# Kernel tuning notes

Hardware: AMD Instinct MI355X
Metric: run time of the kernel (lower is better)

## Reference

```python
import jax, jax.numpy as jnp
import numpy as np

BN = 128  # weight block rows
BK = 128  # quantization block along K
FP8_MAX = 448.0  # float8_e4m3fn max finite value
F8 = jnp.float8_e4m3fn


def _quant_dequant_act(x):
    # Dynamic per-token, per-128-block FP8 quantization (scale = amax/448), then dequant.
    M, K = x.shape
    xb = x.reshape(M, K // BK, BK)
    amax = jnp.max(jnp.abs(xb), axis=-1, keepdims=True)
    scale = jnp.maximum(amax, 1e-12) / FP8_MAX
    q = jnp.clip(xb / scale, -FP8_MAX, FP8_MAX).astype(F8)
    return (q.astype(jnp.float32) * scale).reshape(M, K)


def _dequant_weight(w, s):
    # w: (N, K) fp8, s: (N//BN, K//BK) f32 block scales
    N, K = w.shape
    sf = jnp.repeat(jnp.repeat(s, BN, axis=0), BK, axis=1)[:N, :K]
    return w.astype(jnp.float32) * sf


def _fp8_linear(x, w, s):
    # y = dequant(quant(x)) @ dequant(w)^T  -- matches w8a8_fp8_matmul semantics
    return _quant_dequant_act(x) @ _dequant_weight(w, s).T


def _quantize_weight(key, shape):
    E, N, K = shape
    w = jax.random.normal(key, shape, jnp.float32) * 0.02
    wb = w.reshape(E, N // BN, BN, K // BK, BK)
    amax = jnp.max(jnp.abs(wb), axis=(2, 4), keepdims=True)
    scale = jnp.maximum(amax, 1e-12) / FP8_MAX
    q = jnp.clip(wb / scale, -FP8_MAX, FP8_MAX).astype(F8).reshape(E, N, K)
    return q, scale.reshape(E, N // BN, K // BK)


def setup_inputs() -> dict:
    key = jax.random.key(0)
    k1, k2, k3, k4, k5 = jax.random.split(key, 5)
    T, H, I, E, TOPK = 2048, 2048, 1408, 8, 2
    hidden_states = jax.random.normal(k1, (T, H), jnp.float32)
    top_k_index = jax.random.randint(k2, (T, TOPK), 0, E).astype(jnp.int64)
    w = jax.random.uniform(k3, (T, TOPK), jnp.float32)
    top_k_weights = w / jnp.sum(w, axis=-1, keepdims=True)
    gate_up_proj, gate_up_proj_scale_inv = _quantize_weight(k4, (E, 2 * I, H))
    down_proj, down_proj_scale_inv = _quantize_weight(k5, (E, H, I))
    return {
        "hidden_states": hidden_states,
        "top_k_index": top_k_index,
        "top_k_weights": top_k_weights,
        "gate_up_proj": gate_up_proj,
        "gate_up_proj_scale_inv": gate_up_proj_scale_inv,
        "down_proj": down_proj,
        "down_proj_scale_inv": down_proj_scale_inv,
    }


def reference(hidden_states, top_k_index, top_k_weights, gate_up_proj,
              gate_up_proj_scale_inv, down_proj, down_proj_scale_inv):
    E = gate_up_proj.shape[0]
    I = down_proj.shape[-1]
    # Activation quantization is per-token: identical for every expert, compute once.
    x_dq = _quant_dequant_act(hidden_states)  # (T, H)
    out = jnp.zeros_like(hidden_states, dtype=jnp.float32)
    for e in range(E):  # fixed small expert loop (structural, not data dim)
        gu = x_dq @ _dequant_weight(gate_up_proj[e], gate_up_proj_scale_inv[e]).T  # (T, 2I)
        gate, up = gu[:, :I], gu[:, I:]
        h = jax.nn.silu(gate) * up
        d = _fp8_linear(h, down_proj[e], down_proj_scale_inv[e])  # (T, H)
        # routing weight for this expert per token (sums duplicates like index_add_)
        rw = jnp.sum(jnp.where(top_k_index == e, top_k_weights, 0.0), axis=-1)  # (T,)
        out = out + rw[:, None] * d
    return out.astype(hidden_states.dtype)
```

## Files before the change

kernel.cpp:

```cpp
#include <hip/hip_runtime.h>
#include <cstdint>
#include <cstddef>

using f32x4 = __attribute__((ext_vector_type(4))) float;

#define TDIM 2048
#define HDIM 2048
#define IDIM 1408
#define NEXP 8
#define NKB1 16
#define NKB2 11
#define MAXM 4096

__device__ __forceinline__ void gll16(const void* g, void* l) {
  __builtin_amdgcn_global_load_lds(
      (__attribute__((address_space(1))) void*)(uintptr_t)g,
      (__attribute__((address_space(3))) void*)(uint32_t)(uintptr_t)l,
      16, 0, 0);
}

__device__ __forceinline__ f32x4 mfma_fp8(long a, long b, f32x4 c) {
  return __builtin_amdgcn_mfma_f32_16x16x32_fp8_fp8(a, b, c, 0, 0, 0);
}

__device__ __forceinline__ uint32_t f8_1(float q) {
  q = fminf(fmaxf(q, -448.f), 448.f);
  return (uint32_t)__builtin_amdgcn_cvt_pk_fp8_f32(q, q, 0, false) & 0xffu;
}

__device__ __forceinline__ float bf16_to_f32(uint32_t bits16) {
  union { uint32_t u; float f; } c;
  c.u = bits16 << 16;
  return c.f;
}

__global__ void sniff_kernel(const uint16_t* __restrict__ a,
                             const uint16_t* __restrict__ b,
                             int* __restrict__ modes, int* __restrict__ cnt) {
  if (threadIdx.x < 8) cnt[threadIdx.x] = 0;
  if (threadIdx.x == 0) {
    unsigned acc = 0;
    for (int i = 0; i < 128; ++i) acc |= a[2 * i];
    modes[0] = (acc == 0) ? 1 : 0;
    acc = 0;
    for (int i = 0; i < 128; ++i) acc |= b[2 * i];
    modes[1] = (acc == 0) ? 1 : 0;
  }
}

__global__ void repack_kernel(const void* __restrict__ in, uint8_t* __restrict__ out,
                              int n8, const int* __restrict__ modes, int midx) {
  const int i = blockIdx.x * 256 + threadIdx.x;
  if (i >= n8) return;
  const int m = modes[midx];
  float f[8];
  if (m == 1) {
    const float4* p = (const float4*)in;
    float4 a = p[2 * i], b = p[2 * i + 1];
    f[0] = a.x; f[1] = a.y; f[2] = a.z; f[3] = a.w;
    f[4] = b.x; f[5] = b.y; f[6] = b.z; f[7] = b.w;
  } else {
    uint4 v = ((const uint4*)in)[i];
#pragma unroll
    for (int j = 0; j < 4; ++j) {
      uint32_t w = (&v.x)[j];
      f[2 * j]     = bf16_to_f32(w & 0xffffu);
      f[2 * j + 1] = bf16_to_f32(w >> 16);
    }
  }
  uint32_t lo = 0, hi = 0;
#pragma unroll
  for (int j = 0; j < 8; ++j) {
    uint32_t b8 = f8_1(f[j]);
    if (j < 4) lo |= b8 << (8 * j);
    else       hi |= b8 << (8 * (j - 4));
  }
  ((uint2*)out)[i] = make_uint2(lo, hi);
}

__global__ void quantx_kernel(const float* __restrict__ x,
                              uint8_t* __restrict__ xq, float* __restrict__ xs) {
  const int gid = blockIdx.x * 4 + (threadIdx.x >> 6);
  const int lane = threadIdx.x & 63;
  const int r = gid >> 4, kb = gid & 15;
  const float2 v = *(const float2*)(x + (size_t)r * HDIM + kb * 128 + lane * 2);
  float a = fmaxf(fabsf(v.x), fabsf(v.y));
#pragma unroll
  for (int d = 1; d < 64; d <<= 1) a = fmaxf(a, __shfl_xor(a, d));
  const float s = fmaxf(a, 1e-12f) / 448.f;
  const uint32_t b0 = f8_1(v.x / s);
  const uint32_t b1 = f8_1(v.y / s);
  *(uint16_t*)(xq + (size_t)r * HDIM + kb * 128 + lane * 2) = (uint16_t)(b0 | (b1 << 8));
  if (lane == 0) xs[r * 16 + kb] = s;
}

__global__ void route_kernel(const void* __restrict__ idxraw,
                             int* __restrict__ list, int* __restrict__ cnt) {
  const long long* p = (const long long*)idxraw;
  unsigned hi = 0;
#pragma unroll
  for (int j = 0; j < 16; ++j) hi |= (unsigned)((unsigned long long)p[j] >> 32);
  const int i = blockIdx.x * 256 + threadIdx.x;
  int e;
  if (hi == 0) {
    e = (int)p[i];
  } else {
    long long v = p[i >> 1];
    e = (int)((i & 1) ? (v >> 32) : (v & 0xffffffffLL));
  }
  e &= 7;
  const int pos = atomicAdd(&cnt[e], 1);
  list[e * MAXM + pos] = i;
}

__global__ __launch_bounds__(256) void gemm1_kernel(
    const uint8_t* __restrict__ xq, const float* __restrict__ xs,
    const uint8_t* __restrict__ w, const float* __restrict__ wscl,
    const int* __restrict__ list, const int* __restrict__ cnt,
    uint8_t* __restrict__ hq, float* __restrict__ hs) {
  const int e = blockIdx.z, mt = blockIdx.y, nb = blockIdx.x;
  const int M = cnt[e];
  if (mt * 64 >= M) return;
  __shared__ __align__(16) uint8_t As[8192];
  __shared__ __align__(16) uint8_t Bg[2 * 16384];
  __shared__ __align__(16) uint8_t Bu[2 * 16384];
  __shared__ int slots[64];
  __shared__ __align__(16) float sxsAll[16][64];
  __shared__ __align__(16) float amx[128];
  const int tid = threadIdx.x, lane = tid & 63, wid = tid >> 6;
  const int wr = wid >> 1, wc = wid & 1;
  if (tid < 64) {
    int m = mt * 64 + tid;
    slots[tid] = list[e * MAXM + (m < M ? m : 0)];
  }
  __syncthreads();
  {
    const int r = tid >> 2, q = tid & 3;
    const int tok = slots[r] >> 1;
    f32x4 v = *(const f32x4*)(xs + (size_t)tok * 16 + q * 4);
    sxsAll[q * 4 + 0][r] = v[0];
    sxsAll[q * 4 + 1][r] = v[1];
    sxsAll[q * 4 + 2][r] = v[2];
    sxsAll[q * 4 + 3][r] = v[3];
  }
  const int s = tid >> 3;
  const int cj0 = ((tid & 7) ^ (s & 7)) << 4;
  const long tokA0 = slots[s] >> 1;
  const long tokA1 = slots[s + 32] >> 1;
  const uint8_t* pA0 = xq + tokA0 * HDIM + cj0;
  const uint8_t* pA1 = xq + tokA1 * HDIM + cj0;
  const size_t wb = (size_t)e * (2 * IDIM) * HDIM;
  const uint8_t* pG = w + wb + (size_t)(nb * 128 + s) * HDIM + cj0;
  const uint8_t* pU = w + wb + (size_t)(IDIM + nb * 128 + s) * HDIM + cj0;
  const float* wsg = wscl + (size_t)e * 352 + nb * 16;
  const float* wsu = wsg + 176;
  f32x4 accg[2][4] = {};
  f32x4 accu[2][4] = {};
  const int kbyte = (lane >> 4) << 3;
#define STAGEB(d, kk) { const int ko_ = (kk) << 7; \
    _Pragma("unroll") \
    for (int k = 0; k < 4; ++k) { \
      gll16(pG + (size_t)(k * 32) * HDIM + ko_, Bg + (d) * 16384 + k * 4096 + tid * 16); \
      gll16(pU + (size_t)(k * 32) * HDIM + ko_, Bu + (d) * 16384 + k * 4096 + tid * 16); \
    } }
  f32x4 rA0 = *(const f32x4*)(pA0);
  f32x4 rA1 = *(const f32x4*)(pA1);
  STAGEB(0, 0)
  __syncthreads();
  int cur = 0;
  for (int kb = 0; kb < NKB1; ++kb) {
    *(f32x4*)(As + tid * 16) = rA0;
    *(f32x4*)(As + 4096 + tid * 16) = rA1;
    if (kb + 1 < NKB1) {
      STAGEB(cur ^ 1, kb + 1)
      const int ko = (kb + 1) << 7;
      rA0 = *(const f32x4*)(pA0 + ko);
      rA1 = *(const f32x4*)(pA1 + ko);
    }
    asm volatile("s_waitcnt lgkmcnt(0)" ::: "memory");
    __builtin_amdgcn_s_barrier();
    const float swg = wsg[kb];
    const float swu = wsu[kb];
    const uint8_t* Bgb = Bg + cur * 16384;
    const uint8_t* Bub = Bu + cur * 16384;
    long af[2][4], bgf[4][4], buf_[4][4];
#pragma unroll
    for (int mi = 0; mi < 2; ++mi) {
      const int r = wr * 32 + mi * 16 + (lane & 15);
      const int xr = (r & 7) << 4;
      const uint8_t* bp = As + r * 128;
#pragma unroll
      for (int kc = 0; kc < 4; ++kc)
        af[mi][kc] = *(const long*)(bp + (((kc << 5) + kbyte) ^ xr));
    }
#pragma unroll
    for (int ni = 0; ni < 4; ++ni) {
      const int r = wc * 64 + ni * 16 + (lane & 15);
      const int xr = (r & 7) << 4;
      const uint8_t* bpg = Bgb + r * 128;
      const uint8_t* bpu = Bub + r * 128;
#pragma unroll
      for (int kc = 0; kc < 4; ++kc) {
        bgf[ni][kc] = *(const long*)(bpg + (((kc << 5) + kbyte) ^ xr));
        buf_[ni][kc] = *(const long*)(bpu + (((kc << 5) + kbyte) ^ xr));
      }
    }
    f32x4 sxg[2], sxu[2];
#pragma unroll
    for (int mi = 0; mi < 2; ++mi) {
      f32x4 sx = *(const f32x4*)(&sxsAll[kb][wr * 32 + mi * 16 + ((lane >> 4) << 2)]);
      sxg[mi] = sx * swg;
      sxu[mi] = sx * swu;
    }
    asm volatile("s_waitcnt lgkmcnt(0)" ::: "memory");
    __builtin_amdgcn_sched_barrier(0);
#pragma unroll
    for (int mi = 0; mi < 2; ++mi)
#pragma unroll
      for (int ni = 0; ni < 4; ++ni) {
        f32x4 pg = {0.f, 0.f, 0.f, 0.f};
        f32x4 pu = {0.f, 0.f, 0.f, 0.f};
#pragma unroll
        for (int kc = 0; kc < 4; ++kc) {
          pg = mfma_fp8(af[mi][kc], bgf[ni][kc], pg);
          pu = mfma_fp8(af[mi][kc], buf_[ni][kc], pu);
        }
#pragma unroll
        for (int j = 0; j < 4; ++j) {
          accg[mi][ni][j] += pg[j] * sxg[mi][j];
          accu[mi][ni][j] += pu[j] * sxu[mi][j];
        }
      }
    asm volatile("s_waitcnt vmcnt(0)" ::: "memory");
    __builtin_amdgcn_s_barrier();
    cur ^= 1;
  }
#undef STAGEB
  f32x4 hv[2][4];
  f32x4 rmax[2];
#pragma unroll
  for (int mi = 0; mi < 2; ++mi) {
#pragma unroll
    for (int ni = 0; ni < 4; ++ni)
#pragma unroll
      for (int j = 0; j < 4; ++j) {
        float g = accg[mi][ni][j];
        float u = accu[mi][ni][j];
        float h = (g / (1.f + expf(-g))) * u;
        hv[mi][ni][j] = h;
        float ah = fabsf(h);
        rmax[mi][j] = (ni == 0) ? ah : fmaxf(rmax[mi][j], ah);
      }
#pragma unroll
    for (int d = 1; d < 16; d <<= 1)
#pragma unroll
      for (int j = 0; j < 4; ++j)
        rmax[mi][j] = fmaxf(rmax[mi][j], __shfl_xor(rmax[mi][j], d));
  }
  __syncthreads();
  if ((lane & 15) == 0) {
#pragma unroll
    for (int mi = 0; mi < 2; ++mi)
#pragma unroll
      for (int j = 0; j < 4; ++j) {
        int row = wr * 32 + mi * 16 + ((lane >> 4) << 2) + j;
        amx[row * 2 + wc] = rmax[mi][j];
      }
  }
  __syncthreads();
  const int Mrem = M - mt * 64;
#pragma unroll
  for (int mi = 0; mi < 2; ++mi)
#pragma unroll
    for (int j = 0; j < 4; ++j) {
      const int row = wr * 32 + mi * 16 + ((lane >> 4) << 2) + j;
      float am = fmaxf(amx[row * 2], amx[row * 2 + 1]);
      float sq = fmaxf(am, 1e-12f) / 448.f;
      if (row < Mrem) {
        const int slot = slots[row];
        uint8_t* hp = hq + (size_t)slot * IDIM + nb * 128 + wc * 64 + (lane & 15);
#pragma unroll
        for (int ni = 0; ni < 4; ++ni)
          hp[ni * 16] = (uint8_t)f8_1(hv[mi][ni][j] / sq);
        if (wc == 0 && (lane & 15) == 0) hs[slot * 16 + nb] = sq;
      }
    }
}

__global__ __launch_bounds__(256) void gemm2_kernel(
    const uint8_t* __restrict__ hq, const float* __restrict__ hs,
    const uint8_t* __restrict__ w, const float* __restrict__ wscl,
    const int* __restrict__ list, const int* __restrict__ cnt,
    const float* __restrict__ tkw, float* __restrict__ tmp) {
  const int e = blockIdx.z, mt = blockIdx.y, nt = blockIdx.x;
  const int M = cnt[e];
  if (mt * 128 >= M) return;
  __shared__ __align__(16) uint8_t As[2 * 16384];
  __shared__ __align__(16) uint8_t Bs[2 * 16384];
  __shared__ int slots[128];
  __shared__ float rwl[128];
  __shared__ __align__(16) float sxsAll[16][128];
  const int tid = threadIdx.x, lane = tid & 63, wid = tid >> 6;
  const int wr = wid >> 1, wc = wid & 1;
  if (tid < 128) {
    int m = mt * 128 + tid;
    int slot = list[e * MAXM + (m < M ? m : 0)];
    slots[tid] = slot;
    rwl[tid] = (m < M) ? tkw[slot] : 0.f;
  }
  __syncthreads();
  {
    const int r = tid >> 1, q2 = (tid & 1) * 2;
    const float* ps = hs + (size_t)slots[r] * 16;
#pragma unroll
    for (int qq = 0; qq < 2; ++qq) {
      f32x4 v = *(const f32x4*)(ps + (q2 + qq) * 4);
      sxsAll[(q2 + qq) * 4 + 0][r] = v[0];
      sxsAll[(q2 + qq) * 4 + 1][r] = v[1];
      sxsAll[(q2 + qq) * 4 + 2][r] = v[2];
      sxsAll[(q2 + qq) * 4 + 3][r] = v[3];
    }
  }
  const int s = tid >> 3;
  const int cj0 = ((tid & 7) ^ (s & 7)) << 4;
  const long sA0 = slots[s];
  const long sA1 = slots[s + 32];
  const long sA2 = slots[s + 64];
  const long sA3 = slots[s + 96];
  const uint8_t* pA0 = hq + sA0 * IDIM + cj0;
  const uint8_t* pA1 = hq + sA1 * IDIM + cj0;
  const uint8_t* pA2 = hq + sA2 * IDIM + cj0;
  const uint8_t* pA3 = hq + sA3 * IDIM + cj0;
  const uint8_t* pB = w + (size_t)e * HDIM * IDIM + (size_t)(nt * 128 + s) * IDIM + cj0;
  const float* wsd = wscl + (size_t)e * 176 + nt * 11;
  f32x4 acc[4][4] = {};
  const int kbyte = (lane >> 4) << 3;
#define STAGE2(d, kk) { const int ko_ = (kk) << 7; \
    gll16(pA0 + ko_, As + (d) * 16384 + tid * 16); \
    gll16(pA1 + ko_, As + (d) * 16384 + 4096 + tid * 16); \
    gll16(pA2 + ko_, As + (d) * 16384 + 8192 + tid * 16); \
    gll16(pA3 + ko_, As + (d) * 16384 + 12288 + tid * 16); \
    _Pragma("unroll") \
    for (int k = 0; k < 4; ++k) \
      gll16(pB + (size_t)(k * 32) * IDIM + ko_, Bs + (d) * 16384 + k * 4096 + tid * 16); }
  STAGE2(0, 0)
  __syncthreads();
  int cur = 0;
  for (int kb = 0; kb < NKB2; ++kb) {
    if (kb + 1 < NKB2) STAGE2(cur ^ 1, kb + 1)
    const float swd = wsd[kb];
    const uint8_t* Ab = As + cur * 16384;
    const uint8_t* Bb = Bs + cur * 16384;
    long af[4][4], bf[4][4];
#pragma unroll
    for (int mi = 0; mi < 4; ++mi) {
      const int r = wr * 64 + mi * 16 + (lane & 15);
      const int xr = (r & 7) << 4;
      const uint8_t* bp = Ab + r * 128;
#pragma unroll
      for (int kc = 0; kc < 4; ++kc)
        af[mi][kc] = *(const long*)(bp + (((kc << 5) + kbyte) ^ xr));
    }
#pragma unroll
    for (int ni = 0; ni < 4; ++ni) {
      const int r = wc * 64 + ni * 16 + (lane & 15);
      const int xr = (r & 7) << 4;
      const uint8_t* bp = Bb + r * 128;
#pragma unroll
      for (int kc = 0; kc < 4; ++kc)
        bf[ni][kc] = *(const long*)(bp + (((kc << 5) + kbyte) ^ xr));
    }
    f32x4 sxd[4];
#pragma unroll
    for (int mi = 0; mi < 4; ++mi) {
      f32x4 sx = *(const f32x4*)(&sxsAll[kb][wr * 64 + mi * 16 + ((lane >> 4) << 2)]);
      sxd[mi] = sx * swd;
    }
    asm volatile("s_waitcnt lgkmcnt(0)" ::: "memory");
    __builtin_amdgcn_sched_barrier(0);
#pragma unroll
    for (int mi = 0; mi < 4; ++mi)
#pragma unroll
      for (int ni = 0; ni < 4; ++ni) {
        f32x4 p = {0.f, 0.f, 0.f, 0.f};
#pragma unroll
        for (int kc = 0; kc < 4; ++kc) p = mfma_fp8(af[mi][kc], bf[ni][kc], p);
#pragma unroll
        for (int j = 0; j < 4; ++j) acc[mi][ni][j] += p[j] * sxd[mi][j];
      }
    asm volatile("s_waitcnt vmcnt(0)" ::: "memory");
    __builtin_amdgcn_s_barrier();
    cur ^= 1;
  }
#undef STAGE2
  const int Mrem = M - mt * 128;
#pragma unroll
  for (int mi = 0; mi < 4; ++mi)
#pragma unroll
    for (int j = 0; j < 4; ++j) {
      const int row = wr * 64 + mi * 16 + ((lane >> 4) << 2) + j;
      if (row < Mrem) {
        const int slot = slots[row];
        const float rw = rwl[row];
        float* op = tmp + (size_t)slot * HDIM + nt * 128 + wc * 64 + (lane & 15);
#pragma unroll
        for (int ni = 0; ni < 4; ++ni) op[ni * 16] = rw * acc[mi][ni][j];
      }
    }
}

__global__ void reduce_kernel(const float* __restrict__ tmp, float* __restrict__ out) {
  const int i = blockIdx.x * 256 + threadIdx.x;
  const int t = i >> 9, c4 = i & 511;
  const f32x4 a = ((const f32x4*)tmp)[(size_t)(2 * t) * 512 + c4];
  const f32x4 c = ((const f32x4*)tmp)[(size_t)(2 * t) * 512 + 512 + c4];
  ((f32x4*)out)[i] = a + c;
}

extern "C" void kernel_launch(void* const* d_in, const int* in_sizes, int n_in,
                              void* d_out, int out_size, void* d_ws, size_t ws_size,
                              hipStream_t stream) {
  const float* hidden = (const float*)d_in[0];
  const void* topk_idx = d_in[1];
  const float* topk_w = (const float*)d_in[2];
  const void* gup_raw = d_in[3];
  const float* gup_s = (const float*)d_in[4];
  const void* dwn_raw = d_in[5];
  const float* dwn_s = (const float*)d_in[6];
  float* out = (float*)d_out;
  uint8_t* ws = (uint8_t*)d_ws;
  uint8_t* xq = ws;
  float* xs = (float*)(ws + 4194304);
  uint8_t* hq = ws + 4325376;
  float* hs = (float*)(ws + 10092544);
  int* list = (int*)(ws + 10354688);
  int* cnt = (int*)(ws + 10485760);
  int* modes = (int*)(ws + 10485824);
  uint8_t* gq = ws + 10485888;
  float* tmp = (float*)gq;
  uint8_t* dq = ws + 56623232;
  (void)in_sizes; (void)n_in; (void)ws_size; (void)out_size;

  sniff_kernel<<<1, 64, 0, stream>>>((const uint16_t*)gup_raw, (const uint16_t*)dwn_raw, modes, cnt);
  repack_kernel<<<(5767168 + 255) / 256, 256, 0, stream>>>(gup_raw, gq, 5767168, modes, 0);
  repack_kernel<<<(2883584 + 255) / 256, 256, 0, stream>>>(dwn_raw, dq, 2883584, modes, 1);
  quantx_kernel<<<8192, 256, 0, stream>>>(hidden, xq, xs);
  route_kernel<<<16, 256, 0, stream>>>(topk_idx, list, cnt);
  gemm1_kernel<<<dim3(11, 64, 8), 256, 0, stream>>>(xq, xs, gq, gup_s, list, cnt, hq, hs);
  gemm2_kernel<<<dim3(16, 32, 8), 256, 0, stream>>>(hq, hs, dq, dwn_s, list, cnt, topk_w, tmp);
  reduce_kernel<<<4096, 256, 0, stream>>>(tmp, out);
}
```

Baseline: 226.9 us.

## Split B-tile prefetch into two halves with fine-grained vmcnt waits in both GEMMs

Both grouped GEMM kernels now issue the next K-block's weight prefetch in two halves, each interleaved with half of the current block's MFMA work. Partial vmcnt waits and an extra barrier per iteration replace the single full drain at the end. Loading only half the B fragments at a time also lowers register pressure. The aim is to overlap global-to-LDS loads with compute. The risks are extra barrier overhead, and vmcnt counts that could be wrong if the compiler reorders or adds memory operations.

```diff
diff --git a/kernel.cpp b/kernel.cpp
--- a/kernel.cpp
+++ b/kernel.cpp
@@ -157,33 +157,42 @@
   f32x4 accg[2][4] = {};
   f32x4 accu[2][4] = {};
   const int kbyte = (lane >> 4) << 3;
-#define STAGEB(d, kk) { const int ko_ = (kk) << 7; \
-    _Pragma("unroll") \
-    for (int k = 0; k < 4; ++k) { \
-      gll16(pG + (size_t)(k * 32) * HDIM + ko_, Bg + (d) * 16384 + k * 4096 + tid * 16); \
-      gll16(pU + (size_t)(k * 32) * HDIM + ko_, Bu + (d) * 16384 + k * 4096 + tid * 16); \
-    } }
+#define STAGEB_C0(d, kk) { const int ko_ = (kk) << 7; \
+    gll16(pG + ko_, Bg + (d) * 16384 + tid * 16); \
+    gll16(pG + (size_t)64 * HDIM + ko_, Bg + (d) * 16384 + 8192 + tid * 16); \
+    gll16(pU + ko_, Bu + (d) * 16384 + tid * 16); \
+    gll16(pU + (size_t)64 * HDIM + ko_, Bu + (d) * 16384 + 8192 + tid * 16); }
+#define STAGEB_C1(d, kk) { const int ko_ = (kk) << 7; \
+    gll16(pG + (size_t)32 * HDIM + ko_, Bg + (d) * 16384 + 4096 + tid * 16); \
+    gll16(pG + (size_t)96 * HDIM + ko_, Bg + (d) * 16384 + 12288 + tid * 16); \
+    gll16(pU + (size_t)32 * HDIM + ko_, Bu + (d) * 16384 + 4096 + tid * 16); \
+    gll16(pU + (size_t)96 * HDIM + ko_, Bu + (d) * 16384 + 12288 + tid * 16); }
   f32x4 rA0 = *(const f32x4*)(pA0);
   f32x4 rA1 = *(const f32x4*)(pA1);
-  STAGEB(0, 0)
+  STAGEB_C0(0, 0)
+  STAGEB_C1(0, 0)
   __syncthreads();
   int cur = 0;
   for (int kb = 0; kb < NKB1; ++kb) {
+    asm volatile("s_waitcnt vmcnt(8)" ::: "memory");
     *(f32x4*)(As + tid * 16) = rA0;
     *(f32x4*)(As + 4096 + tid * 16) = rA1;
     if (kb + 1 < NKB1) {
-      STAGEB(cur ^ 1, kb + 1)
       const int ko = (kb + 1) << 7;
       rA0 = *(const f32x4*)(pA0 + ko);
       rA1 = *(const f32x4*)(pA1 + ko);
-    }
-    asm volatile("s_waitcnt lgkmcnt(0)" ::: "memory");
+      STAGEB_C0(cur ^ 1, kb + 1)
+      asm volatile("s_waitcnt lgkmcnt(0) vmcnt(10)" ::: "memory");
+    } else {
+      asm volatile("s_waitcnt lgkmcnt(0) vmcnt(4)" ::: "memory");
+    }
     __builtin_amdgcn_s_barrier();
+    __builtin_amdgcn_sched_barrier(0);
     const float swg = wsg[kb];
     const float swu = wsu[kb];
     const uint8_t* Bgb = Bg + cur * 16384;
     const uint8_t* Bub = Bu + cur * 16384;
-    long af[2][4], bgf[4][4], buf_[4][4];
+    long af[2][4];
 #pragma unroll
     for (int mi = 0; mi < 2; ++mi) {
       const int r = wr * 32 + mi * 16 + (lane & 15);
@@ -193,18 +202,6 @@
       for (int kc = 0; kc < 4; ++kc)
         af[mi][kc] = *(const long*)(bp + (((kc << 5) + kbyte) ^ xr));
     }
-#pragma unroll
-    for (int ni = 0; ni < 4; ++ni) {
-      const int r = wc * 64 + ni * 16 + (lane & 15);
-      const int xr = (r & 7) << 4;
-      const uint8_t* bpg = Bgb + r * 128;
-      const uint8_t* bpu = Bub + r * 128;
-#pragma unroll
-      for (int kc = 0; kc < 4; ++kc) {
-        bgf[ni][kc] = *(const long*)(bpg + (((kc << 5) + kbyte) ^ xr));
-        buf_[ni][kc] = *(const long*)(bpu + (((kc << 5) + kbyte) ^ xr));
-      }
-    }
     f32x4 sxg[2], sxu[2];
 #pragma unroll
     for (int mi = 0; mi < 2; ++mi) {
@@ -212,30 +209,82 @@
       sxg[mi] = sx * swg;
       sxu[mi] = sx * swu;
     }
-    asm volatile("s_waitcnt lgkmcnt(0)" ::: "memory");
+    {
+      long bgf[2][4], buf_[2][4];
+#pragma unroll
+      for (int ni = 0; ni < 2; ++ni) {
+        const int r = wc * 64 + ni * 16 + (lane & 15);
+        const int xr = (r & 7) << 4;
+        const uint8_t* bpg = Bgb + r * 128;
+        const uint8_t* bpu = Bub + r * 128;
+#pragma unroll
+        for (int kc = 0; kc < 4; ++kc) {
+          bgf[ni][kc] = *(const long*)(bpg + (((kc << 5) + kbyte) ^ xr));
+          buf_[ni][kc] = *(const long*)(bpu + (((kc << 5) + kbyte) ^ xr));
+        }
+      }
+#pragma unroll
+      for (int mi = 0; mi < 2; ++mi)
+#pragma unroll
+        for (int ni = 0; ni < 2; ++ni) {
+          f32x4 pg = {0.f, 0.f, 0.f, 0.f};
+          f32x4 pu = {0.f, 0.f, 0.f, 0.f};
+#pragma unroll
+          for (int kc = 0; kc < 4; ++kc) {
+            pg = mfma_fp8(af[mi][kc], bgf[ni][kc], pg);
+            pu = mfma_fp8(af[mi][kc], buf_[ni][kc], pu);
+          }
+#pragma unroll
+          for (int j = 0; j < 4; ++j) {
+            accg[mi][ni][j] += pg[j] * sxg[mi][j];
+            accu[mi][ni][j] += pu[j] * sxu[mi][j];
+          }
+        }
+    }
+    if (kb + 1 < NKB1) {
+      STAGEB_C1(cur ^ 1, kb + 1)
+      asm volatile("s_waitcnt vmcnt(10)" ::: "memory");
+    } else {
+      asm volatile("s_waitcnt vmcnt(0)" ::: "memory");
+    }
+    __builtin_amdgcn_s_barrier();
     __builtin_amdgcn_sched_barrier(0);
-#pragma unroll
-    for (int mi = 0; mi < 2; ++mi)
-#pragma unroll
-      for (int ni = 0; ni < 4; ++ni) {
-        f32x4 pg = {0.f, 0.f, 0.f, 0.f};
-        f32x4 pu = {0.f, 0.f, 0.f, 0.f};
+    {
+      long bgf[2][4], buf_[2][4];
+#pragma unroll
+      for (int ni = 0; ni < 2; ++ni) {
+        const int r = wc * 64 + (ni + 2) * 16 + (lane & 15);
+        const int xr = (r & 7) << 4;
+        const uint8_t* bpg = Bgb + r * 128;
+        const uint8_t* bpu = Bub + r * 128;
 #pragma unroll
         for (int kc = 0; kc < 4; ++kc) {
-          pg = mfma_fp8(af[mi][kc], bgf[ni][kc], pg);
-          pu = mfma_fp8(af[mi][kc], buf_[ni][kc], pu);
+          bgf[ni][kc] = *(const long*)(bpg + (((kc << 5) + kbyte) ^ xr));
+          buf_[ni][kc] = *(const long*)(bpu + (((kc << 5) + kbyte) ^ xr));
         }
-#pragma unroll
-        for (int j = 0; j < 4; ++j) {
-          accg[mi][ni][j] += pg[j] * sxg[mi][j];
-          accu[mi][ni][j] += pu[j] * sxu[mi][j];
+      }
+#pragma unroll
+      for (int mi = 0; mi < 2; ++mi)
+#pragma unroll
+        for (int ni = 0; ni < 2; ++ni) {
+          f32x4 pg = {0.f, 0.f, 0.f, 0.f};
+          f32x4 pu = {0.f, 0.f, 0.f, 0.f};
+#pragma unroll
+          for (int kc = 0; kc < 4; ++kc) {
+            pg = mfma_fp8(af[mi][kc], bgf[ni][kc], pg);
+            pu = mfma_fp8(af[mi][kc], buf_[ni][kc], pu);
+          }
+#pragma unroll
+          for (int j = 0; j < 4; ++j) {
+            accg[mi][ni + 2][j] += pg[j] * sxg[mi][j];
+            accu[mi][ni + 2][j] += pu[j] * sxu[mi][j];
+          }
         }
-      }
-    asm volatile("s_waitcnt vmcnt(0)" ::: "memory");
-    __builtin_amdgcn_s_barrier();
+    }
     cur ^= 1;
   }
-#undef STAGEB
+#undef STAGEB_C0
+#undef STAGEB_C1
   f32x4 hv[2][4];
   f32x4 rmax[2];
 #pragma unroll
@@ -335,23 +384,36 @@
   const float* wsd = wscl + (size_t)e * 176 + nt * 11;
   f32x4 acc[4][4] = {};
   const int kbyte = (lane >> 4) << 3;
-#define STAGE2(d, kk) { const int ko_ = (kk) << 7; \
+#define STAGE_A2(d, kk) { const int ko_ = (kk) << 7; \
     gll16(pA0 + ko_, As + (d) * 16384 + tid * 16); \
     gll16(pA1 + ko_, As + (d) * 16384 + 4096 + tid * 16); \
     gll16(pA2 + ko_, As + (d) * 16384 + 8192 + tid * 16); \
-    gll16(pA3 + ko_, As + (d) * 16384 + 12288 + tid * 16); \
-    _Pragma("unroll") \
-    for (int k = 0; k < 4; ++k) \
-      gll16(pB + (size_t)(k * 32) * IDIM + ko_, Bs + (d) * 16384 + k * 4096 + tid * 16); }
-  STAGE2(0, 0)
+    gll16(pA3 + ko_, As + (d) * 16384 + 12288 + tid * 16); }
+#define STAGE_B2C0(d, kk) { const int ko_ = (kk) << 7; \
+    gll16(pB + ko_, Bs + (d) * 16384 + tid * 16); \
+    gll16(pB + (size_t)64 * IDIM + ko_, Bs + (d) * 16384 + 8192 + tid * 16); }
+#define STAGE_B2C1(d, kk) { const int ko_ = (kk) << 7; \
+    gll16(pB + (size_t)32 * IDIM + ko_, Bs + (d) * 16384 + 4096 + tid * 16); \
+    gll16(pB + (size_t)96 * IDIM + ko_, Bs + (d) * 16384 + 12288 + tid * 16); }
+  STAGE_A2(0, 0)
+  STAGE_B2C0(0, 0)
+  STAGE_B2C1(0, 0)
   __syncthreads();
   int cur = 0;
   for (int kb = 0; kb < NKB2; ++kb) {
-    if (kb + 1 < NKB2) STAGE2(cur ^ 1, kb + 1)
-    const float swd = wsd[kb];
     const uint8_t* Ab = As + cur * 16384;
     const uint8_t* Bb = Bs + cur * 16384;
-    long af[4][4], bf[4][4];
+    if (kb + 1 < NKB2) {
+      STAGE_A2(cur ^ 1, kb + 1)
+      STAGE_B2C0(cur ^ 1, kb + 1)
+      asm volatile("s_waitcnt vmcnt(8)" ::: "memory");
+    } else {
+      asm volatile("s_waitcnt vmcnt(2)" ::: "memory");
+    }
+    __builtin_amdgcn_s_barrier();
+    __builtin_amdgcn_sched_barrier(0);
+    const float swd = wsd[kb];
+    long af[4][4];
 #pragma unroll
     for (int mi = 0; mi < 4; ++mi) {
       const int r = wr * 64 + mi * 16 + (lane & 15);
@@ -361,38 +423,69 @@
       for (int kc = 0; kc < 4; ++kc)
         af[mi][kc] = *(const long*)(bp + (((kc << 5) + kbyte) ^ xr));
     }
-#pragma unroll
-    for (int ni = 0; ni < 4; ++ni) {
-      const int r = wc * 64 + ni * 16 + (lane & 15);
-      const int xr = (r & 7) << 4;
-      const uint8_t* bp = Bb + r * 128;
-#pragma unroll
-      for (int kc = 0; kc < 4; ++kc)
-        bf[ni][kc] = *(const long*)(bp + (((kc << 5) + kbyte) ^ xr));
-    }
     f32x4 sxd[4];
 #pragma unroll
     for (int mi = 0; mi < 4; ++mi) {
       f32x4 sx = *(const f32x4*)(&sxsAll[kb][wr * 64 + mi * 16 + ((lane >> 4) << 2)]);
       sxd[mi] = sx * swd;
     }
-    asm volatile("s_waitcnt lgkmcnt(0)" ::: "memory");
+    {
+      long bf[2][4];
+#pragma unroll
+      for (int ni = 0; ni < 2; ++ni) {
+        const int r = wc * 64 + ni * 16 + (lane & 15);
+        const int xr = (r & 7) << 4;
+        const uint8_t* bp = Bb + r * 128;
+#pragma unroll
+        for (int kc = 0; kc < 4; ++kc)
+          bf[ni][kc] = *(const long*)(bp + (((kc << 5) + kbyte) ^ xr));
+      }
+#pragma unroll
+      for (int mi = 0; mi < 4; ++mi)
+#pragma unroll
+        for (int ni = 0; ni < 2; ++ni) {
+          f32x4 p = {0.f, 0.f, 0.f, 0.f};
+#pragma unroll
+          for (int kc = 0; kc < 4; ++kc) p = mfma_fp8(af[mi][kc], bf[ni][kc], p);
+#pragma unroll
+          for (int j = 0; j < 4; ++j) acc[mi][ni][j] += p[j] * sxd[mi][j];
+        }
+    }
+    if (kb + 1 < NKB2) {
+      STAGE_B2C1(cur ^ 1, kb + 1)
+      asm volatile("s_waitcnt vmcnt(8)" ::: "memory");
+    } else {
+      asm volatile("s_waitcnt vmcnt(0)" ::: "memory");
+    }
+    __builtin_amdgcn_s_barrier();
     __builtin_amdgcn_sched_barrier(0);
-#pragma unroll
-    for (int mi = 0; mi < 4; ++mi)
-#pragma unroll
-      for (int ni = 0; ni < 4; ++ni) {
-        f32x4 p = {0.f, 0.f, 0.f, 0.f};
-#pragma unroll
-        for (int kc = 0; kc < 4; ++kc) p = mfma_fp8(af[mi][kc], bf[ni][kc], p);
-#pragma unroll
-        for (int j = 0; j < 4; ++j) acc[mi][ni][j] += p[j] * sxd[mi][j];
-      }
-    asm volatile("s_waitcnt vmcnt(0)" ::: "memory");
-    __builtin_amdgcn_s_barrier();
+    {
+      long bf[2][4];
+#pragma unroll
+      for (int ni = 0; ni < 2; ++ni) {
+        const int r = wc * 64 + (ni + 2) * 16 + (lane & 15);
+        const int xr = (r & 7) << 4;
+        const uint8_t* bp = Bb + r * 128;
+#pragma unroll
+        for (int kc = 0; kc < 4; ++kc)
+          bf[ni][kc] = *(const long*)(bp + (((kc << 5) + kbyte) ^ xr));
+      }
+#pragma unroll
+      for (int mi = 0; mi < 4; ++mi)
+#pragma unroll
+        for (int ni = 0; ni < 2; ++ni) {
+          f32x4 p = {0.f, 0.f, 0.f, 0.f};
+#pragma unroll
+          for (int kc = 0; kc < 4; ++kc) p = mfma_fp8(af[mi][kc], bf[ni][kc], p);
+#pragma unroll
+          for (int j = 0; j < 4; ++j) acc[mi][ni + 2][j] += p[j] * sxd[mi][j];
+        }
+    }
     cur ^= 1;
   }
-#undef STAGE2
+#undef STAGE_A2
+#undef STAGE_B2C0
+#undef STAGE_B2C1
   const int Mrem = M - mt * 128;
 #pragma unroll
   for (int mi = 0; mi < 4; ++mi)
```

New measurement: 239.8 us. +5.7%, slower.

## Halve gemm2 M tile to 64 and stage A through registers

Applied to the files above, without the earlier changes.

The down-projection GEMM now uses 64-row M tiles instead of 128, doubling the grid's M dimension so more workgroups run and fewer padded rows are wasted on partially filled expert tiles. The A operand is no longer loaded with direct global-to-LDS copies. It is prefetched into registers and written into a single LDS buffer each iteration, with an extra barrier. This cuts LDS and register use, but B weight tiles are reused over fewer rows, so weight traffic roughly doubles and each iteration pays one more synchronisation.

```diff
diff --git a/kernel.cpp b/kernel.cpp
--- a/kernel.cpp
+++ b/kernel.cpp
@@ -294,69 +294,68 @@
     const float* __restrict__ tkw, float* __restrict__ tmp) {
   const int e = blockIdx.z, mt = blockIdx.y, nt = blockIdx.x;
   const int M = cnt[e];
-  if (mt * 128 >= M) return;
-  __shared__ __align__(16) uint8_t As[2 * 16384];
+  if (mt * 64 >= M) return;
+  __shared__ __align__(16) uint8_t As[8192];
   __shared__ __align__(16) uint8_t Bs[2 * 16384];
-  __shared__ int slots[128];
-  __shared__ float rwl[128];
-  __shared__ __align__(16) float sxsAll[16][128];
+  __shared__ int slots[64];
+  __shared__ float rwl[64];
+  __shared__ __align__(16) float sxsAll[16][64];
   const int tid = threadIdx.x, lane = tid & 63, wid = tid >> 6;
   const int wr = wid >> 1, wc = wid & 1;
-  if (tid < 128) {
-    int m = mt * 128 + tid;
+  if (tid < 64) {
+    int m = mt * 64 + tid;
     int slot = list[e * MAXM + (m < M ? m : 0)];
     slots[tid] = slot;
     rwl[tid] = (m < M) ? tkw[slot] : 0.f;
   }
   __syncthreads();
   {
-    const int r = tid >> 1, q2 = (tid & 1) * 2;
+    const int r = tid >> 2, q = tid & 3;
     const float* ps = hs + (size_t)slots[r] * 16;
-#pragma unroll
-    for (int qq = 0; qq < 2; ++qq) {
-      f32x4 v = *(const f32x4*)(ps + (q2 + qq) * 4);
-      sxsAll[(q2 + qq) * 4 + 0][r] = v[0];
-      sxsAll[(q2 + qq) * 4 + 1][r] = v[1];
-      sxsAll[(q2 + qq) * 4 + 2][r] = v[2];
-      sxsAll[(q2 + qq) * 4 + 3][r] = v[3];
-    }
+    f32x4 v = *(const f32x4*)(ps + q * 4);
+    sxsAll[q * 4 + 0][r] = v[0];
+    sxsAll[q * 4 + 1][r] = v[1];
+    sxsAll[q * 4 + 2][r] = v[2];
+    sxsAll[q * 4 + 3][r] = v[3];
   }
   const int s = tid >> 3;
   const int cj0 = ((tid & 7) ^ (s & 7)) << 4;
   const long sA0 = slots[s];
   const long sA1 = slots[s + 32];
-  const long sA2 = slots[s + 64];
-  const long sA3 = slots[s + 96];
   const uint8_t* pA0 = hq + sA0 * IDIM + cj0;
   const uint8_t* pA1 = hq + sA1 * IDIM + cj0;
-  const uint8_t* pA2 = hq + sA2 * IDIM + cj0;
-  const uint8_t* pA3 = hq + sA3 * IDIM + cj0;
   const uint8_t* pB = w + (size_t)e * HDIM * IDIM + (size_t)(nt * 128 + s) * IDIM + cj0;
   const float* wsd = wscl + (size_t)e * 176 + nt * 11;
-  f32x4 acc[4][4] = {};
+  f32x4 acc[2][4] = {};
   const int kbyte = (lane >> 4) << 3;
-#define STAGE2(d, kk) { const int ko_ = (kk) << 7; \
-    gll16(pA0 + ko_, As + (d) * 16384 + tid * 16); \
-    gll16(pA1 + ko_, As + (d) * 16384 + 4096 + tid * 16); \
-    gll16(pA2 + ko_, As + (d) * 16384 + 8192 + tid * 16); \
-    gll16(pA3 + ko_, As + (d) * 16384 + 12288 + tid * 16); \
+#define STAGEB2(d, kk) { const int ko_ = (kk) << 7; \
     _Pragma("unroll") \
     for (int k = 0; k < 4; ++k) \
       gll16(pB + (size_t)(k * 32) * IDIM + ko_, Bs + (d) * 16384 + k * 4096 + tid * 16); }
-  STAGE2(0, 0)
+  f32x4 rA0 = *(const f32x4*)(pA0);
+  f32x4 rA1 = *(const f32x4*)(pA1);
+  STAGEB2(0, 0)
   __syncthreads();
   int cur = 0;
   for (int kb = 0; kb < NKB2; ++kb) {
-    if (kb + 1 < NKB2) STAGE2(cur ^ 1, kb + 1)
+    *(f32x4*)(As + tid * 16) = rA0;
+    *(f32x4*)(As + 4096 + tid * 16) = rA1;
+    if (kb + 1 < NKB2) {
+      STAGEB2(cur ^ 1, kb + 1)
+      const int ko = (kb + 1) << 7;
+      rA0 = *(const f32x4*)(pA0 + ko);
+      rA1 = *(const f32x4*)(pA1 + ko);
+    }
+    asm volatile("s_waitcnt lgkmcnt(0)" ::: "memory");
+    __builtin_amdgcn_s_barrier();
     const float swd = wsd[kb];
-    const uint8_t* Ab = As + cur * 16384;
     const uint8_t* Bb = Bs + cur * 16384;
-    long af[4][4], bf[4][4];
-#pragma unroll
-    for (int mi = 0; mi < 4; ++mi) {
-      const int r = wr * 64 + mi * 16 + (lane & 15);
+    long af[2][4], bf[4][4];
+#pragma unroll
+    for (int mi = 0; mi < 2; ++mi) {
+      const int r = wr * 32 + mi * 16 + (lane & 15);
       const int xr = (r & 7) << 4;
-      const uint8_t* bp = Ab + r * 128;
+      const uint8_t* bp = As + r * 128;
 #pragma unroll
       for (int kc = 0; kc < 4; ++kc)
         af[mi][kc] = *(const long*)(bp + (((kc << 5) + kbyte) ^ xr));
@@ -370,16 +369,16 @@
       for (int kc = 0; kc < 4; ++kc)
         bf[ni][kc] = *(const long*)(bp + (((kc << 5) + kbyte) ^ xr));
     }
-    f32x4 sxd[4];
-#pragma unroll
-    for (int mi = 0; mi < 4; ++mi) {
-      f32x4 sx = *(const f32x4*)(&sxsAll[kb][wr * 64 + mi * 16 + ((lane >> 4) << 2)]);
+    f32x4 sxd[2];
+#pragma unroll
+    for (int mi = 0; mi < 2; ++mi) {
+      f32x4 sx = *(const f32x4*)(&sxsAll[kb][wr * 32 + mi * 16 + ((lane >> 4) << 2)]);
       sxd[mi] = sx * swd;
     }
     asm volatile("s_waitcnt lgkmcnt(0)" ::: "memory");
     __builtin_amdgcn_sched_barrier(0);
 #pragma unroll
-    for (int mi = 0; mi < 4; ++mi)
+    for (int mi = 0; mi < 2; ++mi)
 #pragma unroll
       for (int ni = 0; ni < 4; ++ni) {
         f32x4 p = {0.f, 0.f, 0.f, 0.f};
@@ -392,13 +391,13 @@
     __builtin_amdgcn_s_barrier();
     cur ^= 1;
   }
-#undef STAGE2
-  const int Mrem = M - mt * 128;
-#pragma unroll
-  for (int mi = 0; mi < 4; ++mi)
+#undef STAGEB2
+  const int Mrem = M - mt * 64;
+#pragma unroll
+  for (int mi = 0; mi < 2; ++mi)
 #pragma unroll
     for (int j = 0; j < 4; ++j) {
-      const int row = wr * 64 + mi * 16 + ((lane >> 4) << 2) + j;
+      const int row = wr * 32 + mi * 16 + ((lane >> 4) << 2) + j;
       if (row < Mrem) {
         const int slot = slots[row];
         const float rw = rwl[row];
@@ -447,6 +446,6 @@
   quantx_kernel<<<8192, 256, 0, stream>>>(hidden, xq, xs);
   route_kernel<<<16, 256, 0, stream>>>(topk_idx, list, cnt);
   gemm1_kernel<<<dim3(11, 64, 8), 256, 0, stream>>>(xq, xs, gq, gup_s, list, cnt, hq, hs);
-  gemm2_kernel<<<dim3(16, 32, 8), 256, 0, stream>>>(hq, hs, dq, dwn_s, list, cnt, topk_w, tmp);
+  gemm2_kernel<<<dim3(16, 64, 8), 256, 0, stream>>>(hq, hs, dq, dwn_s, list, cnt, topk_w, tmp);
   reduce_kernel<<<4096, 256, 0, stream>>>(tmp, out);
 }
```

New measurement: 225.3 us. About the same (-0.7%).
